# Kernel optimization log

Hardware: AMD Instinct MI355X
Metric: run time of the kernel (lower is better)

Reference implementation:

```python
import jax, jax.numpy as jnp
import numpy as np

D_IN = 1024
D_OUT = 1024

def setup_inputs() -> dict:
    key = jax.random.key(0)
    k1, k2, k3, k4 = jax.random.split(key, 4)
    x = jax.random.normal(k1, (4, 2048, D_IN), dtype=jnp.float32)
    s = 1.0 / np.sqrt(D_IN)
    Wk = jax.random.normal(k2, (D_OUT, D_IN), dtype=jnp.float32) * s
    Wq = jax.random.normal(k3, (D_OUT, D_IN), dtype=jnp.float32) * s
    Wv = jax.random.normal(k4, (D_OUT, D_IN), dtype=jnp.float32) * s
    return {"x": x, "Wk": Wk, "Wq": Wq, "Wv": Wv}

def reference(x, Wk, Wq, Wv):
    # Note: original code applies k_w to produce 'weighted_q' and q_w for
    # 'weighted_k' (swapped names); we reproduce the exact math.
    b, s, _ = x.shape
    q = jnp.einsum('bsd,ed->bse', x, Wk)  # [B,S,d_out]
    k = jnp.einsum('bsd,ed->bse', x, Wq)  # [B,S,d_out]
    v = jnp.einsum('bsd,ed->bse', x, Wv)  # [B,S,d_out]
    scores = jnp.einsum('bqe,bke->bqk', q, k)  # [B,S,S]
    causal = jnp.triu(jnp.ones((s, s), dtype=bool), k=1)  # True = masked (future)
    scores = jnp.where(causal[None], -jnp.inf, scores)
    inv_sqrt_d = jnp.float32(1.0 / np.sqrt(Wk.shape[0]))
    attn = jax.nn.softmax(scores * inv_sqrt_d, axis=-1)
    return jnp.einsum('bqk,bke->bqe', attn, v)
```

## Files before the change

### kernel.cpp

```cpp
#include <hip/hip_runtime.h>
#include <hip/hip_bf16.h>
#include <stdint.h>

#define BATCH 4
#define SEQ   2048
#define DIN   1024
#define DOUT  1024
#define MTOT  (BATCH*SEQ)

typedef __attribute__((ext_vector_type(8))) short bf16x8;
typedef __attribute__((ext_vector_type(4))) float f32x4;

__device__ inline unsigned short f2bf(float f) {
  union { float f; unsigned u; } a; a.f = f;
  unsigned r = a.u + 0x7fffu + ((a.u >> 16) & 1u);
  return (unsigned short)(r >> 16);
}

__device__ inline void gload_lds16(const void* g, void* l) {
  __builtin_amdgcn_global_load_lds(
      (__attribute__((address_space(1))) void*)(uintptr_t)(g),
      (__attribute__((address_space(3))) void*)(uintptr_t)(l),
      16, 0, 0);
}

__global__ __launch_bounds__(256)
void convert_kernel(const float* __restrict__ x, const float* __restrict__ wk,
                    const float* __restrict__ wq, const float* __restrict__ wv,
                    unsigned short* __restrict__ xb, unsigned short* __restrict__ wkqb,
                    unsigned short* __restrict__ wvb) {
  const long NX = (long)MTOT * DIN;
  const long NW = (long)DOUT * DIN;
  long t = (long)blockIdx.x * blockDim.x + threadIdx.x;
  long off = t * 4;
  if (off >= NX + 3 * NW) return;
  const float* src; unsigned short* dst; long o;
  if (off < NX)            { src = x;  dst = xb;        o = off; }
  else if (off < NX + NW)  { src = wk; dst = wkqb;      o = off - NX; }
  else if (off < NX + 2*NW){ src = wq; dst = wkqb + NW; o = off - NX - NW; }
  else                     { src = wv; dst = wvb;       o = off - NX - 2*NW; }
  f32x4 v = *(const f32x4*)(src + o);
  unsigned p0 = (unsigned)f2bf(v[0]) | ((unsigned)f2bf(v[1]) << 16);
  unsigned p1 = (unsigned)f2bf(v[2]) | ((unsigned)f2bf(v[3]) << 16);
  uint2* d = (uint2*)(dst + o);
  *d = make_uint2(p0, p1);
}

#define BM 128
#define BN 128
#define BK 64

__global__ __launch_bounds__(256, 2)
void gemm_kernel(const unsigned short* __restrict__ A,
                 const unsigned short* __restrict__ Bw,
                 void* __restrict__ Cout,
                 int lda, int ldb, int ldc, int K,
                 long aBatch, long bBatch, long cBatch,
                 float scale, int outBf16, int tri, int klimit) {
  int bj = blockIdx.x, bi = blockIdx.y, b = blockIdx.z;
  if (tri && bj > bi) return;
  int Keff = K;
  if (klimit) { int km = (bi + 1) * BM; Keff = km < K ? km : K; }

  const unsigned short* Ab = A  + (long)b * aBatch + (long)bi * BM * lda;
  const unsigned short* Bb = Bw + (long)b * bBatch + (long)bj * BN * ldb;

  __shared__ unsigned short at[BM * BK];
  __shared__ unsigned short bt[BN * BK];

  const int tid  = threadIdx.x;
  const int lane = tid & 63;
  const int w    = tid >> 6;
  const int wm   = w >> 1;
  const int wn   = w & 1;

  f32x4 acc[4][4];
#pragma unroll
  for (int i = 0; i < 4; i++)
#pragma unroll
    for (int j = 0; j < 4; j++) acc[i][j] = (f32x4){0.f, 0.f, 0.f, 0.f};

  const int srow = lane >> 3;
  const int scol = (lane & 7) * 8;

  const int ntiles = Keff / BK;
  for (int kt = 0; kt < ntiles; ++kt) {
    const int k0 = kt * BK;
    if (kt) __syncthreads();
#pragma unroll
    for (int t = 0; t < 4; t++) {
      const int r = w * 32 + t * 8 + srow;
      gload_lds16(Ab + (long)r * lda + k0 + scol, &at[(w * 32 + t * 8) * BK + lane * 8]);
      gload_lds16(Bb + (long)r * ldb + k0 + scol, &bt[(w * 32 + t * 8) * BK + lane * 8]);
    }
    asm volatile("s_waitcnt vmcnt(0)" ::: "memory");
    __syncthreads();
#pragma unroll
    for (int kk = 0; kk < 2; ++kk) {
      bf16x8 af[4], bfr[4];
#pragma unroll
      for (int i = 0; i < 4; i++)
        af[i] = *(const bf16x8*)&at[(wm * 64 + i * 16 + (lane & 15)) * BK + kk * 32 + (lane >> 4) * 8];
#pragma unroll
      for (int j = 0; j < 4; j++)
        bfr[j] = *(const bf16x8*)&bt[(wn * 64 + j * 16 + (lane & 15)) * BK + kk * 32 + (lane >> 4) * 8];
#pragma unroll
      for (int i = 0; i < 4; i++)
#pragma unroll
        for (int j = 0; j < 4; j++)
          acc[i][j] = __builtin_amdgcn_mfma_f32_16x16x32_bf16(af[i], bfr[j], acc[i][j], 0, 0, 0);
    }
  }

  const long crow0 = (long)bi * BM + wm * 64;
  const long ccol0 = (long)bj * BN + wn * 64;
  if (outBf16) {
    unsigned short* C = (unsigned short*)Cout + (long)b * cBatch;
#pragma unroll
    for (int i = 0; i < 4; i++) {
      const long row0 = crow0 + i * 16 + ((lane >> 4) << 2);
#pragma unroll
      for (int j = 0; j < 4; j++) {
        const long col = ccol0 + j * 16 + (lane & 15);
#pragma unroll
        for (int r2 = 0; r2 < 4; r2++)
          C[(row0 + r2) * ldc + col] = f2bf(acc[i][j][r2] * scale);
      }
    }
  } else {
    float* C = (float*)Cout + (long)b * cBatch;
#pragma unroll
    for (int i = 0; i < 4; i++) {
      const long row0 = crow0 + i * 16 + ((lane >> 4) << 2);
#pragma unroll
      for (int j = 0; j < 4; j++) {
        const long col = ccol0 + j * 16 + (lane & 15);
#pragma unroll
        for (int r2 = 0; r2 < 4; r2++)
          C[(row0 + r2) * ldc + col] = acc[i][j][r2] * scale;
      }
    }
  }
}

__global__ __launch_bounds__(256)
void softmax_kernel(const float* __restrict__ scores, unsigned short* __restrict__ P) {
  __shared__ float rowbuf[SEQ];
  __shared__ float red[8];
  const int r = blockIdx.x;
  const int i = r & (SEQ - 1);
  const int n = i + 1;
  const int kend = ((i >> 7) + 1) << 7;
  const float* src = scores + (long)r * SEQ;
  unsigned short* dst = P + (long)r * SEQ;
  const int tid = threadIdx.x;

  float m = -1e30f;
  for (int j = tid; j < n; j += 256) { float v = src[j]; rowbuf[j] = v; m = fmaxf(m, v); }
#pragma unroll
  for (int o = 32; o; o >>= 1) m = fmaxf(m, __shfl_down(m, o, 64));
  if ((tid & 63) == 0) red[tid >> 6] = m;
  __syncthreads();
  m = fmaxf(fmaxf(red[0], red[1]), fmaxf(red[2], red[3]));

  float s = 0.f;
  for (int j = tid; j < n; j += 256) { float e = __expf(rowbuf[j] - m); rowbuf[j] = e; s += e; }
#pragma unroll
  for (int o = 32; o; o >>= 1) s += __shfl_down(s, o, 64);
  if ((tid & 63) == 0) red[4 + (tid >> 6)] = s;
  __syncthreads();
  s = red[4] + red[5] + red[6] + red[7];
  const float inv = 1.0f / s;

  for (int j = tid; j < n; j += 256) dst[j] = f2bf(rowbuf[j] * inv);
  for (int j = n + tid; j < kend; j += 256) dst[j] = 0;
}

extern "C" void kernel_launch(void* const* d_in, const int* in_sizes, int n_in,
                              void* d_out, int out_size, void* d_ws, size_t ws_size,
                              hipStream_t stream) {
  const float* x  = (const float*)d_in[0];
  const float* Wk = (const float*)d_in[1];
  const float* Wq = (const float*)d_in[2];
  const float* Wv = (const float*)d_in[3];

  char* ws = (char*)d_ws;
  unsigned short* xb   = (unsigned short*)(ws);
  unsigned short* qk   = (unsigned short*)(ws + 16777216);
  unsigned short* vtb  = (unsigned short*)(ws + 50331648);
  unsigned short* wkqb = (unsigned short*)(ws + 67108864);
  unsigned short* wvb  = (unsigned short*)(ws + 71303168);
  float*          scores = (float*)(ws + 73400320);
  unsigned short* P    = (unsigned short*)(ws + 140509184);
  float* out = (float*)d_out;

  {
    long total4 = ((long)MTOT * DIN + 3L * DOUT * DIN) / 4;
    int blocks = (int)((total4 + 255) / 256);
    convert_kernel<<<dim3(blocks), dim3(256), 0, stream>>>(x, Wk, Wq, Wv, xb, wkqb, wvb);
  }
  gemm_kernel<<<dim3(2048 / BN, 8192 / BM, 1), dim3(256), 0, stream>>>(
      xb, wkqb, qk, 1024, 1024, 2048, 1024, 0L, 0L, 0L, 1.0f, 1, 0, 0);
  gemm_kernel<<<dim3(8192 / BN, 1024 / BM, 1), dim3(256), 0, stream>>>(
      wvb, xb, vtb, 1024, 1024, 8192, 1024, 0L, 0L, 0L, 1.0f, 1, 0, 0);
  gemm_kernel<<<dim3(16, 16, BATCH), dim3(256), 0, stream>>>(
      qk, qk + 1024, scores, 2048, 2048, 2048, 1024,
      (long)SEQ * 2048, (long)SEQ * 2048, (long)SEQ * SEQ, 0.03125f, 0, 1, 0);
  softmax_kernel<<<dim3(BATCH * SEQ), dim3(256), 0, stream>>>(scores, P);
  gemm_kernel<<<dim3(1024 / BN, 2048 / BM, BATCH), dim3(256), 0, stream>>>(
      P, vtb, out, 2048, 8192, 1024, 2048,
      (long)SEQ * SEQ, 2048L, (long)SEQ * DOUT, 1.0f, 0, 0, 1);
}
```

Before: 287.8 us.

## Add double-buffered 256x256 GEMM for QK projection, bf16 scores, packed triangular grid

Adds a 256x256-tile GEMM kernel with 512 threads, double-buffered LDS and MFMA priority hints, and uses it for the fused Q/K projection to get more operand reuse and overlap loads with compute. The scores GEMM now writes bf16 instead of fp32, halving scores traffic into softmax. It also launches only lower-triangular tiles through a packed 1D index, so no blocks are spent just exiting. Bf16 scores lose some precision before softmax, and the larger tile uses 128KB of LDS, which limits occupancy.

```diff
diff --git a/kernel.cpp b/kernel.cpp
--- a/kernel.cpp
+++ b/kernel.cpp
@@ -15,6 +15,9 @@
   union { float f; unsigned u; } a; a.f = f;
   unsigned r = a.u + 0x7fffu + ((a.u >> 16) & 1u);
   return (unsigned short)(r >> 16);
+}
+__device__ inline float bf2f(unsigned short b) {
+  union { unsigned u; float f; } a; a.u = ((unsigned)b) << 16; return a.f;
 }
 
 __device__ inline void gload_lds16(const void* g, void* l) {
@@ -46,6 +49,110 @@
   *d = make_uint2(p0, p1);
 }
 
+#define TBM 256
+#define TBN 256
+#define TBK 64
+
+__global__ __launch_bounds__(512, 2)
+void gemm256_kernel(const unsigned short* __restrict__ A,
+                    const unsigned short* __restrict__ Bw,
+                    unsigned short* __restrict__ C,
+                    int lda, int ldb, int ldc, int K) {
+  const int bj = blockIdx.x, bi = blockIdx.y;
+  const unsigned short* Ab = A + (long)bi * TBM * lda;
+  const unsigned short* Bb = Bw + (long)bj * TBN * ldb;
+
+  __shared__ unsigned short at[2][TBM * TBK];
+  __shared__ unsigned short bt[2][TBN * TBK];
+
+  const int tid  = threadIdx.x;
+  const int lane = tid & 63;
+  const int w    = tid >> 6;
+  const int wm   = w >> 2;
+  const int wn   = w & 3;
+
+  f32x4 acc[8][4];
+#pragma unroll
+  for (int i = 0; i < 8; i++)
+#pragma unroll
+    for (int j = 0; j < 4; j++) acc[i][j] = (f32x4){0.f, 0.f, 0.f, 0.f};
+
+  const int srow = lane >> 3;
+  const int scol = (lane & 7) * 8;
+
+  const int nt = K / TBK;
+
+#define STAGE256(buf, kt)                                                          \
+  {                                                                                \
+    const int k0 = (kt) * TBK;                                                     \
+    _Pragma("unroll")                                                              \
+    for (int c = 0; c < 4; c++) {                                                  \
+      const int rr = (w * 4 + c) * 8;                                              \
+      gload_lds16(Ab + (long)(rr + srow) * lda + k0 + scol,                        \
+                  &at[buf][rr * TBK + lane * 8]);                                  \
+    }                                                                              \
+    _Pragma("unroll")                                                              \
+    for (int c = 0; c < 4; c++) {                                                  \
+      const int rr = (w * 4 + c) * 8;                                              \
+      gload_lds16(Bb + (long)(rr + srow) * ldb + k0 + scol,                        \
+                  &bt[buf][rr * TBK + lane * 8]);                                  \
+    }                                                                              \
+  }
+
+#define COMPUTE256(buf)                                                            \
+  {                                                                                \
+    _Pragma("unroll")                                                              \
+    for (int kk = 0; kk < 2; kk++) {                                               \
+      bf16x8 af[8], bfr[4];                                                        \
+      _Pragma("unroll")                                                            \
+      for (int i = 0; i < 8; i++)                                                  \
+        af[i] = *(const bf16x8*)&at[buf][(wm * 128 + i * 16 + (lane & 15)) * TBK   \
+                                         + kk * 32 + (lane >> 4) * 8];             \
+      _Pragma("unroll")                                                            \
+      for (int j = 0; j < 4; j++)                                                  \
+        bfr[j] = *(const bf16x8*)&bt[buf][(wn * 64 + j * 16 + (lane & 15)) * TBK   \
+                                          + kk * 32 + (lane >> 4) * 8];            \
+      __builtin_amdgcn_s_setprio(1);                                               \
+      _Pragma("unroll")                                                            \
+      for (int i = 0; i < 8; i++)                                                  \
+        _Pragma("unroll")                                                          \
+        for (int j = 0; j < 4; j++)                                                \
+          acc[i][j] = __builtin_amdgcn_mfma_f32_16x16x32_bf16(af[i], bfr[j],       \
+                                                              acc[i][j], 0, 0, 0); \
+      __builtin_amdgcn_s_setprio(0);                                               \
+    }                                                                              \
+  }
+
+  STAGE256(0, 0);
+  asm volatile("s_waitcnt vmcnt(0)" ::: "memory");
+  __syncthreads();
+
+  for (int kt = 0; kt < nt - 1; ++kt) {
+    const int cur = kt & 1;
+    STAGE256(cur ^ 1, kt + 1);
+    COMPUTE256(cur);
+    asm volatile("s_waitcnt vmcnt(0)" ::: "memory");
+    __syncthreads();
+  }
+  COMPUTE256((nt - 1) & 1);
+
+  const long crow0 = (long)bi * TBM + wm * 128;
+  const long ccol0 = (long)bj * TBN + wn * 64;
+#pragma unroll
+  for (int i = 0; i < 8; i++) {
+    const long row0 = crow0 + i * 16 + ((lane >> 4) << 2);
+#pragma unroll
+    for (int j = 0; j < 4; j++) {
+      const long col = ccol0 + j * 16 + (lane & 15);
+#pragma unroll
+      for (int r2 = 0; r2 < 4; r2++)
+        C[(row0 + r2) * ldc + col] = f2bf(acc[i][j][r2]);
+    }
+  }
+#undef STAGE256
+#undef COMPUTE256
+}
+
 #define BM 128
 #define BN 128
 #define BK 64
@@ -56,9 +163,15 @@
                  void* __restrict__ Cout,
                  int lda, int ldb, int ldc, int K,
                  long aBatch, long bBatch, long cBatch,
-                 float scale, int outBf16, int tri, int klimit) {
+                 float scale, int outBf16, int triPack, int klimit) {
   int bj = blockIdx.x, bi = blockIdx.y, b = blockIdx.z;
-  if (tri && bj > bi) return;
+  if (triPack) {
+    int idx = blockIdx.x;
+    int t = (int)((sqrtf(8.f * idx + 1.f) - 1.f) * 0.5f);
+    while ((t + 1) * (t + 2) / 2 <= idx) t++;
+    while (t * (t + 1) / 2 > idx) t--;
+    bi = t; bj = idx - t * (t + 1) / 2;
+  }
   int Keff = K;
   if (klimit) { int km = (bi + 1) * BM; Keff = km < K ? km : K; }
 
@@ -144,19 +257,19 @@
 }
 
 __global__ __launch_bounds__(256)
-void softmax_kernel(const float* __restrict__ scores, unsigned short* __restrict__ P) {
+void softmax_kernel(const unsigned short* __restrict__ scores, unsigned short* __restrict__ P) {
   __shared__ float rowbuf[SEQ];
   __shared__ float red[8];
   const int r = blockIdx.x;
   const int i = r & (SEQ - 1);
   const int n = i + 1;
   const int kend = ((i >> 7) + 1) << 7;
-  const float* src = scores + (long)r * SEQ;
+  const unsigned short* src = scores + (long)r * SEQ;
   unsigned short* dst = P + (long)r * SEQ;
   const int tid = threadIdx.x;
 
   float m = -1e30f;
-  for (int j = tid; j < n; j += 256) { float v = src[j]; rowbuf[j] = v; m = fmaxf(m, v); }
+  for (int j = tid; j < n; j += 256) { float v = bf2f(src[j]); rowbuf[j] = v; m = fmaxf(m, v); }
 #pragma unroll
   for (int o = 32; o; o >>= 1) m = fmaxf(m, __shfl_down(m, o, 64));
   if ((tid & 63) == 0) red[tid >> 6] = m;
@@ -185,13 +298,13 @@
   const float* Wv = (const float*)d_in[3];
 
   char* ws = (char*)d_ws;
-  unsigned short* xb   = (unsigned short*)(ws);
-  unsigned short* qk   = (unsigned short*)(ws + 16777216);
-  unsigned short* vtb  = (unsigned short*)(ws + 50331648);
-  unsigned short* wkqb = (unsigned short*)(ws + 67108864);
-  unsigned short* wvb  = (unsigned short*)(ws + 71303168);
-  float*          scores = (float*)(ws + 73400320);
-  unsigned short* P    = (unsigned short*)(ws + 140509184);
+  unsigned short* xb      = (unsigned short*)(ws);
+  unsigned short* qk      = (unsigned short*)(ws + 16777216);
+  unsigned short* vtb     = (unsigned short*)(ws + 50331648);
+  unsigned short* wkqb    = (unsigned short*)(ws + 67108864);
+  unsigned short* wvb     = (unsigned short*)(ws + 71303168);
+  unsigned short* scoresb = (unsigned short*)(ws + 73400320);
+  unsigned short* P       = (unsigned short*)(ws + 106954752);
   float* out = (float*)d_out;
 
   {
@@ -199,14 +312,14 @@
     int blocks = (int)((total4 + 255) / 256);
     convert_kernel<<<dim3(blocks), dim3(256), 0, stream>>>(x, Wk, Wq, Wv, xb, wkqb, wvb);
   }
-  gemm_kernel<<<dim3(2048 / BN, 8192 / BM, 1), dim3(256), 0, stream>>>(
-      xb, wkqb, qk, 1024, 1024, 2048, 1024, 0L, 0L, 0L, 1.0f, 1, 0, 0);
+  gemm256_kernel<<<dim3(2048 / TBN, 8192 / TBM), dim3(512), 0, stream>>>(
+      xb, wkqb, qk, 1024, 1024, 2048, 1024);
   gemm_kernel<<<dim3(8192 / BN, 1024 / BM, 1), dim3(256), 0, stream>>>(
       wvb, xb, vtb, 1024, 1024, 8192, 1024, 0L, 0L, 0L, 1.0f, 1, 0, 0);
-  gemm_kernel<<<dim3(16, 16, BATCH), dim3(256), 0, stream>>>(
-      qk, qk + 1024, scores, 2048, 2048, 2048, 1024,
-      (long)SEQ * 2048, (long)SEQ * 2048, (long)SEQ * SEQ, 0.03125f, 0, 1, 0);
-  softmax_kernel<<<dim3(BATCH * SEQ), dim3(256), 0, stream>>>(scores, P);
+  gemm_kernel<<<dim3(136, 1, BATCH), dim3(256), 0, stream>>>(
+      qk, qk + 1024, scoresb, 2048, 2048, 2048, 1024,
+      (long)SEQ * 2048, (long)SEQ * 2048, (long)SEQ * SEQ, 0.03125f, 1, 1, 0);
+  softmax_kernel<<<dim3(BATCH * SEQ), dim3(256), 0, stream>>>(scoresb, P);
   gemm_kernel<<<dim3(1024 / BN, 2048 / BM, BATCH), dim3(256), 0, stream>>>(
       P, vtb, out, 2048, 8192, 1024, 2048,
       (long)SEQ * SEQ, 2048L, (long)SEQ * DOUT, 1.0f, 0, 0, 1);
```

Result: faster. 265.9 us (-7.6%).
